# Optimization experiments

Measured on AMD Instinct MI355X. Metric: run time of the kernel, lower is better.

The kernel has to match this reference:

```python
import jax, jax.numpy as jnp
import numpy as np

N_NODES = 20000
N_EDGES = 320000
N_GRAPHS = 64


def gat_conv(x, src, dst, W, a_src, a_dst, bias, heads, ch, concat):
    # x: [N, F_in]; W: [F_in, heads*ch]; a_src/a_dst: [heads, ch]
    N = x.shape[0]
    h = (x @ W).reshape(N, heads, ch)                       # [N, H, C]
    alpha_s = jnp.sum(h * a_src, axis=-1)                   # [N, H]
    alpha_d = jnp.sum(h * a_dst, axis=-1)                   # [N, H]
    e = jax.nn.leaky_relu(alpha_s[src] + alpha_d[dst], 0.2) # [E, H]
    # segment softmax over incoming edges of each destination node
    m = jax.ops.segment_max(e, dst, num_segments=N)         # [N, H]
    ex = jnp.exp(e - m[dst])
    denom = jax.ops.segment_sum(ex, dst, num_segments=N)    # [N, H]
    alpha = ex / (denom[dst] + 1e-16)                       # [E, H]
    msg = h[src] * alpha[:, :, None]                        # [E, H, C]
    out = jax.ops.segment_sum(msg, dst, num_segments=N)     # [N, H, C]
    out = out.reshape(N, heads * ch) if concat else out.mean(axis=1)
    return out + bias, alpha


def setup_inputs() -> dict:
    key = jax.random.key(0)
    ks = jax.random.split(key, 24)
    dim_in, md, dim_out = 8, 64, 128
    hid = md * 4  # 256
    p = lambda k, shape: jax.random.normal(k, shape, dtype=jnp.float32) * 0.1
    inp = {
        "x_ppi": jax.random.normal(ks[0], (N_NODES, dim_in), dtype=jnp.float32),
        "ppi_edge_index": jax.random.randint(ks[1], (2, N_EDGES), 0, N_NODES),
        "ppi_batch": jnp.sort(jax.random.randint(ks[2], (N_NODES,), 0, N_GRAPHS)),
        # GATConv 1: dim_in -> 64, heads=4, concat
        "W1": p(ks[3], (dim_in, 4 * md)), "a_src1": p(ks[4], (4, md)), "a_dst1": p(ks[5], (4, md)), "b_gat1": jnp.zeros((hid,), jnp.float32),
        "lw1": p(ks[6], (dim_in, hid)), "lb1": jnp.zeros((hid,), jnp.float32),
        # GATConv 2: 256 -> 64, heads=4, concat
        "W2": p(ks[7], (hid, 4 * md)), "a_src2": p(ks[8], (4, md)), "a_dst2": p(ks[9], (4, md)), "b_gat2": jnp.zeros((hid,), jnp.float32),
        "lw2": p(ks[10], (hid, hid)), "lb2": jnp.zeros((hid,), jnp.float32),
        # GATConv 3: 256 -> 128, heads=6, concat=False (mean)
        "W3": p(ks[11], (hid, 6 * dim_out)), "a_src3": p(ks[12], (6, dim_out)), "a_dst3": p(ks[13], (6, dim_out)), "b_gat3": jnp.zeros((dim_out,), jnp.float32),
        "lw3": p(ks[14], (hid, dim_out)), "lb3": jnp.zeros((dim_out,), jnp.float32),
        # BatchNorm1d(dim_out), training-mode batch statistics
        "bn_gamma": jnp.ones((dim_out,), jnp.float32), "bn_beta": jnp.zeros((dim_out,), jnp.float32),
    }
    return inp


def reference(x_ppi, ppi_edge_index, ppi_batch,
              W1, a_src1, a_dst1, b_gat1, lw1, lb1,
              W2, a_src2, a_dst2, b_gat2, lw2, lb2,
              W3, a_src3, a_dst3, b_gat3, lw3, lb3,
              bn_gamma, bn_beta):
    src, dst = ppi_edge_index[0], ppi_edge_index[1]
    g1, _ = gat_conv(x_ppi, src, dst, W1, a_src1, a_dst1, b_gat1, heads=4, ch=64, concat=True)
    x = jax.nn.relu(g1 + x_ppi @ lw1 + lb1)
    g2, _ = gat_conv(x, src, dst, W2, a_src2, a_dst2, b_gat2, heads=4, ch=64, concat=True)
    x = jax.nn.relu(g2 + x @ lw2 + lb2)
    x_res = x @ lw3 + lb3
    g3, att = gat_conv(x, src, dst, W3, a_src3, a_dst3, b_gat3, heads=6, ch=128, concat=False)
    x = g3 + x_res
    x = jax.nn.relu(x)
    # BatchNorm1d, training mode (biased variance, eps=1e-5)
    mu = x.mean(axis=0)
    var = jnp.mean((x - mu) ** 2, axis=0)
    x = (x - mu) * jax.lax.rsqrt(var + 1e-5) * bn_gamma + bn_beta
    # global max pool over graphs
    pooled = jax.ops.segment_max(x, ppi_batch, num_segments=N_GRAPHS)
    return pooled, att
```

## Files before the change

### kernel.cpp

```cpp
#include <hip/hip_runtime.h>
#include <hip/hip_bf16.h>
#include <math.h>

#define N_NODES 20000
#define N_EDGES 320000
#define N_GRAPHS 64

typedef __bf16 bf16_t;
typedef bf16_t bf16x8 __attribute__((ext_vector_type(8)));
typedef bf16_t bf16x4 __attribute__((ext_vector_type(4)));
typedef bf16_t bf16x2 __attribute__((ext_vector_type(2)));
typedef float f32x4 __attribute__((ext_vector_type(4)));
typedef float f32x2 __attribute__((ext_vector_type(2)));

__global__ void hist_k(const int* __restrict__ dst, int* __restrict__ deg, int E) {
    int e = blockIdx.x * 256 + threadIdx.x;
    if (e < E) atomicAdd(&deg[dst[e]], 1);
}

__global__ __launch_bounds__(1024) void scan_k(const int* __restrict__ deg,
                                               int* __restrict__ offs,
                                               int* __restrict__ cursor, int n) {
    __shared__ int s_ws[16];
    int tid = threadIdx.x;
    int lane = tid & 63, w = tid >> 6;
    int carry = 0;
    for (int base = 0; base < n; base += 1024) {
        int i = base + tid;
        int v = (i < n) ? deg[i] : 0;
        int x = v;
        #pragma unroll
        for (int off = 1; off < 64; off <<= 1) {
            int t = __shfl_up(x, off);
            if (lane >= off) x += t;
        }
        if (lane == 63) s_ws[w] = x;
        __syncthreads();
        if (tid < 16) {
            int y = s_ws[tid];
            #pragma unroll
            for (int off = 1; off < 16; off <<= 1) {
                int t = __shfl_up(y, off);
                if (tid >= off) y += t;
            }
            s_ws[tid] = y;
        }
        __syncthreads();
        int wbase = (w > 0) ? s_ws[w - 1] : 0;
        int ex = carry + wbase + x - v;
        if (i < n) { offs[i] = ex; cursor[i] = ex; }
        carry += s_ws[15];
        __syncthreads();
    }
    if (tid == 0) offs[n] = carry;
}

__global__ void scatter_k(const int* __restrict__ src, const int* __restrict__ dst,
                          int* __restrict__ cursor, int* __restrict__ csr_src,
                          int* __restrict__ csr_eid, int E) {
    int e = blockIdx.x * 256 + threadIdx.x;
    if (e < E) {
        int d = dst[e];
        int p = atomicAdd(&cursor[d], 1);
        csr_src[p] = src[e];
        csr_eid[p] = e;
    }
}

__global__ __launch_bounds__(256) void wt_k(const float* __restrict__ W,
                                            bf16_t* __restrict__ Bt, int K, int N) {
    __shared__ float t[32][33];
    int k0 = blockIdx.y * 32, n0 = blockIdx.x * 32;
    int tx = threadIdx.x & 31, ty = threadIdx.x >> 5;
    for (int i = ty; i < 32; i += 8) t[i][tx] = W[(size_t)(k0 + i) * N + n0 + tx];
    __syncthreads();
    for (int i = ty; i < 32; i += 8)
        Bt[(size_t)(n0 + i) * K + k0 + tx] = (bf16_t)t[tx][i];
}

__global__ void w3s_k(const float* __restrict__ W3, const float* __restrict__ lw3,
                      bf16_t* __restrict__ Bt) {
    int id = blockIdx.x * 256 + threadIdx.x;
    if (id >= 128 * 1792) return;
    int n = id / 1792, k = id - n * 1792;
    float v;
    if (k < 1536) {
        int h = k >> 8, c = k & 255;
        v = W3[(size_t)c * 768 + h * 128 + n] * (1.f / 6.f);
    } else {
        int c = k - 1536;
        v = lw3[(size_t)c * 128 + n];
    }
    Bt[id] = (bf16_t)v;
}

__global__ void b40_k(const float* __restrict__ W1, const float* __restrict__ lw1,
                      float* __restrict__ B) {
    int id = blockIdx.x * 256 + threadIdx.x;
    if (id >= 40 * 256) return;
    int k = id >> 8, n = id & 255;
    float v;
    if (k < 32) {
        int h = k >> 3, c = k & 7;
        v = ((n >> 6) == h) ? W1[(size_t)c * 256 + n] : 0.f;
    } else {
        int c = k - 32;
        v = lw1[(size_t)c * 256 + n];
    }
    B[id] = v;
}

__global__ void va_k(const float* __restrict__ W, const float* __restrict__ a_s,
                     const float* __restrict__ a_d, float* __restrict__ Va,
                     float* __restrict__ Vd, int H, int C) {
    int k = blockIdx.x;
    int lane = threadIdx.x;
    const float* wr = W + (size_t)k * H * C;
    for (int h = 0; h < H; ++h) {
        float sa = 0.f, sd = 0.f;
        for (int c = lane; c < C; c += 64) {
            float wv = wr[h * C + c];
            sa += wv * a_s[h * C + c];
            sd += wv * a_d[h * C + c];
        }
        #pragma unroll
        for (int m = 32; m; m >>= 1) { sa += __shfl_xor(sa, m); sd += __shfl_xor(sd, m); }
        if (lane == 0) { Va[k * H + h] = sa; Vd[k * H + h] = sd; }
    }
}

__global__ void addb_k(const float* __restrict__ a, const float* __restrict__ b,
                       float* __restrict__ o, int n) {
    int i = blockIdx.x * 256 + threadIdx.x;
    if (i < n) o[i] = a[i] + b[i];
}

template <typename OUT>
__global__ __launch_bounds__(256) void gemm_k(const float* __restrict__ A,
                                              const float* __restrict__ B,
                                              OUT* __restrict__ C,
                                              const float* __restrict__ bias,
                                              int M, int N, int K, int relu) {
    __shared__ float As[16][65];
    __shared__ float Bs[16][64];
    int tid = threadIdx.x;
    int tx = tid & 15, ty = tid >> 4;
    int row0 = blockIdx.y * 64, col0 = blockIdx.x * 64;
    float acc[4][4] = {};
    for (int k0 = 0; k0 < K; k0 += 16) {
        #pragma unroll
        for (int i = 0; i < 4; ++i) {
            int idx = tid + i * 256;
            int m = idx >> 4, kk = idx & 15;
            int gm = row0 + m, gk = k0 + kk;
            As[kk][m] = (gm < M && gk < K) ? A[(size_t)gm * K + gk] : 0.f;
        }
        #pragma unroll
        for (int i = 0; i < 4; ++i) {
            int idx = tid + i * 256;
            int kk = idx >> 6, n = idx & 63;
            int gk = k0 + kk, gn = col0 + n;
            Bs[kk][n] = (gk < K && gn < N) ? B[(size_t)gk * N + gn] : 0.f;
        }
        __syncthreads();
        #pragma unroll
        for (int kk = 0; kk < 16; ++kk) {
            float a[4], b[4];
            #pragma unroll
            for (int i = 0; i < 4; ++i) a[i] = As[kk][ty * 4 + i];
            #pragma unroll
            for (int j = 0; j < 4; ++j) b[j] = Bs[kk][tx * 4 + j];
            #pragma unroll
            for (int i = 0; i < 4; ++i)
                #pragma unroll
                for (int j = 0; j < 4; ++j) acc[i][j] += a[i] * b[j];
        }
        __syncthreads();
    }
    #pragma unroll
    for (int i = 0; i < 4; ++i) {
        int gm = row0 + ty * 4 + i;
        if (gm >= M) continue;
        #pragma unroll
        for (int j = 0; j < 4; ++j) {
            int gn = col0 + tx * 4 + j;
            if (gn < N) {
                float r = acc[i][j] + (bias ? bias[gn] : 0.f);
                if (relu) r = fmaxf(r, 0.f);
                C[(size_t)gm * N + gn] = (OUT)r;
            }
        }
    }
}

template <typename OUT>
__global__ __launch_bounds__(256) void gemm_bf16_k(
    const bf16_t* __restrict__ A, const bf16_t* __restrict__ Bt,
    OUT* __restrict__ C, const float* __restrict__ bias, int M, int N, int K,
    const float* __restrict__ asv, const float* __restrict__ adv,
    float* __restrict__ as_o, float* __restrict__ ad_o, int H, int Ch, int relu) {
    __shared__ bf16_t As[128][40];
    __shared__ bf16_t Bs[128][40];
    int tid = threadIdx.x;
    int row0 = blockIdx.y * 128, col0 = blockIdx.x * 128;
    int wave = tid >> 6, lane = tid & 63, quad = lane >> 4, l16 = lane & 15;
    int wm = wave >> 1, wn = wave & 1;
    f32x4 acc[4][4] = {};
    int sr = tid >> 2;
    int sc = (tid & 3) * 8;
    for (int k0 = 0; k0 < K; k0 += 32) {
        #pragma unroll
        for (int half = 0; half < 2; ++half) {
            int r = sr + half * 64;
            int gm = row0 + r;
            bf16x8 v = {};
            if (gm < M) v = *(const bf16x8*)&A[(size_t)gm * K + k0 + sc];
            *(bf16x8*)&As[r][sc] = v;
            int gn = col0 + r;
            bf16x8 w = {};
            if (gn < N) w = *(const bf16x8*)&Bt[(size_t)gn * K + k0 + sc];
            *(bf16x8*)&Bs[r][sc] = w;
        }
        __syncthreads();
        bf16x8 af[4], bfr[4];
        #pragma unroll
        for (int i = 0; i < 4; ++i) {
            af[i] = *(const bf16x8*)&As[wm * 64 + i * 16 + l16][quad * 8];
            bfr[i] = *(const bf16x8*)&Bs[wn * 64 + i * 16 + l16][quad * 8];
        }
        #pragma unroll
        for (int i = 0; i < 4; ++i)
            #pragma unroll
            for (int j = 0; j < 4; ++j)
                acc[i][j] = __builtin_amdgcn_mfma_f32_16x16x32_bf16(af[i], bfr[j],
                                                                   acc[i][j], 0, 0, 0);
        __syncthreads();
    }
    #pragma unroll
    for (int i = 0; i < 4; ++i) {
        int base_m = row0 + wm * 64 + i * 16 + quad * 4;
        #pragma unroll
        for (int j = 0; j < 4; ++j) {
            int gn = col0 + wn * 64 + j * 16 + l16;
            float bv = bias ? bias[gn] : 0.f;
            #pragma unroll
            for (int r = 0; r < 4; ++r) {
                int gm = base_m + r;
                if (gm < M) {
                    float rr = acc[i][j][r] + bv;
                    if (relu) rr = fmaxf(rr, 0.f);
                    C[(size_t)gm * N + gn] = (OUT)rr;
                }
            }
        }
    }
    if (asv) {
        int hd = (col0 + wn * 64) / Ch;
        float av[4], dv[4];
        #pragma unroll
        for (int j = 0; j < 4; ++j) {
            int ca = col0 + wn * 64 + j * 16 + l16;
            av[j] = asv[ca];
            dv[j] = adv[ca];
        }
        #pragma unroll
        for (int i = 0; i < 4; ++i) {
            float sp[4] = {}, sd[4] = {};
            #pragma unroll
            for (int j = 0; j < 4; ++j)
                #pragma unroll
                for (int r = 0; r < 4; ++r) {
                    sp[r] += acc[i][j][r] * av[j];
                    sd[r] += acc[i][j][r] * dv[j];
                }
            #pragma unroll
            for (int m = 1; m < 16; m <<= 1)
                #pragma unroll
                for (int r = 0; r < 4; ++r) {
                    sp[r] += __shfl_xor(sp[r], m);
                    sd[r] += __shfl_xor(sd[r], m);
                }
            if (l16 == 0) {
                #pragma unroll
                for (int r = 0; r < 4; ++r) {
                    int gm = row0 + wm * 64 + i * 16 + quad * 4 + r;
                    if (gm < M) {
                        as_o[gm * H + hd] = sp[r];
                        ad_o[gm * H + hd] = sd[r];
                    }
                }
            }
        }
    }
}

__device__ __forceinline__ float leaky02(float v) { return v > 0.f ? v : 0.2f * v; }

__global__ void asad1_k(const float* __restrict__ x, const float* __restrict__ Va,
                        const float* __restrict__ Vd, float* __restrict__ as_,
                        float* __restrict__ ad_, int N) {
    int idx = blockIdx.x * 256 + threadIdx.x;
    if (idx >= N * 4) return;
    int j = idx >> 2, h = idx & 3;
    const float* xr = x + (size_t)j * 8;
    float sa = 0.f, sd = 0.f;
    #pragma unroll
    for (int c = 0; c < 8; ++c) {
        sa += xr[c] * Va[c * 4 + h];
        sd += xr[c] * Vd[c * 4 + h];
    }
    as_[idx] = sa;
    ad_[idx] = sd;
}

__global__ void asad3_k(const bf16_t* __restrict__ xb, const float* __restrict__ Va,
                        const float* __restrict__ Vd, float* __restrict__ as_,
                        float* __restrict__ ad_) {
    int j = blockIdx.x;
    int lane = threadIdx.x;
    bf16x4 v = *(const bf16x4*)&xb[(size_t)j * 256 + lane * 4];
    float sa[6] = {}, sd[6] = {};
    #pragma unroll
    for (int i = 0; i < 4; ++i) {
        int k = lane * 4 + i;
        float xv = (float)v[i];
        #pragma unroll
        for (int h = 0; h < 6; ++h) {
            sa[h] += xv * Va[k * 6 + h];
            sd[h] += xv * Vd[k * 6 + h];
        }
    }
    #pragma unroll
    for (int h = 0; h < 6; ++h) {
        float a = sa[h], d = sd[h];
        #pragma unroll
        for (int m = 32; m; m >>= 1) { a += __shfl_xor(a, m); d += __shfl_xor(d, m); }
        if (lane == 0) { as_[j * 6 + h] = a; ad_[j * 6 + h] = d; }
    }
}

__global__ __launch_bounds__(256) void agg_z1_k(
    const float* __restrict__ x, const float* __restrict__ as_,
    const float* __restrict__ ad_, const int* __restrict__ offs,
    const int* __restrict__ csr_src, float* __restrict__ z1) {
    int j = blockIdx.x * 4 + (threadIdx.x >> 6);
    int t = threadIdx.x & 63;
    int e_l = t >> 3, c = t & 7;
    int o0 = offs[j], deg = offs[j + 1] - o0;
    float adj0 = ad_[j * 4 + 0], adj1 = ad_[j * 4 + 1];
    float adj2 = ad_[j * 4 + 2], adj3 = ad_[j * 4 + 3];
    float acc[4] = {}, ws[4] = {};
    for (int e0 = 0; e0 < deg; e0 += 8) {
        int ne = min(8, deg - e0);
        if (e_l < ne) {
            int s = csr_src[o0 + e0 + e_l];
            float xv = x[(size_t)s * 8 + c];
            f32x4 a = *(const f32x4*)&as_[s * 4];
            float w0 = __expf(leaky02(a[0] + adj0));
            float w1 = __expf(leaky02(a[1] + adj1));
            float w2 = __expf(leaky02(a[2] + adj2));
            float w3 = __expf(leaky02(a[3] + adj3));
            acc[0] += w0 * xv; acc[1] += w1 * xv;
            acc[2] += w2 * xv; acc[3] += w3 * xv;
            ws[0] += w0; ws[1] += w1; ws[2] += w2; ws[3] += w3;
        }
    }
    #pragma unroll
    for (int m = 8; m < 64; m <<= 1)
        #pragma unroll
        for (int h = 0; h < 4; ++h) {
            acc[h] += __shfl_xor(acc[h], m);
            ws[h] += __shfl_xor(ws[h], m);
        }
    if (e_l == 0) {
        #pragma unroll
        for (int h = 0; h < 4; ++h)
            z1[(size_t)j * 40 + h * 8 + c] = acc[h] / (ws[h] + 1e-16f);
        z1[(size_t)j * 40 + 32 + c] = x[(size_t)j * 8 + c];
    }
}

__global__ __launch_bounds__(256) void agg_concat_k(
    const bf16_t* __restrict__ h, const float* __restrict__ as_,
    const float* __restrict__ ad_, const int* __restrict__ offs,
    const int* __restrict__ csr_src, const float* __restrict__ lin,
    const float* __restrict__ bgat, bf16_t* __restrict__ xb) {
    int j = blockIdx.x;
    int tid = threadIdx.x;
    int o0 = offs[j], deg = offs[j + 1] - o0;
    __shared__ int s_src[64];
    __shared__ float s_adj[4];
    __shared__ float s_ws[8][4];
    __shared__ float s_inv[4];
    __shared__ float s_red[8][256];
    if (tid < 4) s_adj[tid] = ad_[j * 4 + tid];
    int g = tid >> 5;
    int u = tid & 31;
    int myh = u >> 3;
    const char* hbase = (const char*)h + u * 16;
    f32x4 acc0 = {}, acc1 = {};
    float wsum = 0.f;
    for (int e0 = 0; e0 < deg; e0 += 64) {
        int ne = min(64, deg - e0);
        if (tid < ne) s_src[tid] = csr_src[o0 + e0 + tid];
        __syncthreads();
        float adj = s_adj[myh];
        #pragma unroll 2
        for (int e = g; e < ne; e += 8) {
            int s = s_src[e];
            float w = __expf(leaky02(as_[s * 4 + myh] + adj));
            bf16x8 v = *(const bf16x8*)(hbase + (size_t)s * 512);
            wsum += w;
            #pragma unroll
            for (int i = 0; i < 4; ++i) acc0[i] += w * (float)v[i];
            #pragma unroll
            for (int i = 0; i < 4; ++i) acc1[i] += w * (float)v[4 + i];
        }
        __syncthreads();
    }
    if ((u & 7) == 0) s_ws[g][myh] = wsum;
    *(f32x4*)&s_red[g][u * 8] = acc0;
    *(f32x4*)&s_red[g][u * 8 + 4] = acc1;
    __syncthreads();
    if (tid < 4) {
        float d = 0.f;
        #pragma unroll
        for (int g2 = 0; g2 < 8; ++g2) d += s_ws[g2][tid];
        s_inv[tid] = 1.f / (d + 1e-16f);
    }
    __syncthreads();
    {
        int c = tid;
        float s = 0.f;
        #pragma unroll
        for (int g2 = 0; g2 < 8; ++g2) s += s_red[g2][c];
        float v = fmaxf(s * s_inv[c >> 6] + bgat[c] + lin[(size_t)j * 256 + c], 0.f);
        xb[(size_t)j * 256 + c] = (bf16_t)v;
    }
}

__global__ __launch_bounds__(256) void agg_z3_k(
    const bf16_t* __restrict__ xb, const float* __restrict__ as_,
    const float* __restrict__ ad_, const int* __restrict__ offs,
    const int* __restrict__ csr_src, const int* __restrict__ csr_eid,
    bf16_t* __restrict__ z, float* __restrict__ att) {
    int j = blockIdx.x;
    int tid = threadIdx.x;
    int o0 = offs[j], deg = offs[j + 1] - o0;
    __shared__ float s_adj[6], s_denom[6], s_inv[6];
    __shared__ int s_src[64];
    __shared__ float s_w[64 * 6];
    __shared__ float s_red[8][6][256];
    if (tid < 6) { s_adj[tid] = ad_[j * 6 + tid]; s_denom[tid] = 0.f; }
    __syncthreads();
    int g = tid >> 5;
    int c = tid & 31;
    const char* xbase = (const char*)xb + c * 16;
    f32x4 a0[6] = {}, a1[6] = {};
    for (int e0 = 0; e0 < deg; e0 += 64) {
        int ne = min(64, deg - e0);
        #pragma unroll
        for (int base = 0; base < 2; ++base) {
            int idx = tid + base * 256;
            if (idx < ne * 6) {
                int e = idx / 6, h = idx - e * 6;
                int s = csr_src[o0 + e0 + e];
                if (h == 0) s_src[e] = s;
                s_w[idx] = __expf(leaky02(as_[s * 6 + h] + s_adj[h]));
            }
        }
        __syncthreads();
        if (tid < 6) {
            float d = 0.f;
            for (int e = 0; e < ne; ++e) d += s_w[e * 6 + tid];
            s_denom[tid] += d;
        }
        for (int e = g; e < ne; e += 8) {
            int s = s_src[e];
            bf16x8 v = *(const bf16x8*)(xbase + (size_t)s * 512);
            float f0[4], f1[4];
            #pragma unroll
            for (int i = 0; i < 4; ++i) { f0[i] = (float)v[i]; f1[i] = (float)v[4 + i]; }
            #pragma unroll
            for (int h = 0; h < 6; ++h) {
                float w = s_w[e * 6 + h];
                #pragma unroll
                for (int i = 0; i < 4; ++i) {
                    a0[h][i] += w * f0[i];
                    a1[h][i] += w * f1[i];
                }
            }
        }
        __syncthreads();
    }
    #pragma unroll
    for (int h = 0; h < 6; ++h) {
        *(f32x4*)&s_red[g][h][c * 8] = a0[h];
        *(f32x4*)&s_red[g][h][c * 8 + 4] = a1[h];
    }
    if (tid < 6) s_inv[tid] = 1.f / (s_denom[tid] + 1e-16f);
    __syncthreads();
    {
        int cc = tid;
        #pragma unroll
        for (int h = 0; h < 6; ++h) {
            float s = 0.f;
            #pragma unroll
            for (int g2 = 0; g2 < 8; ++g2) s += s_red[g2][h][cc];
            z[(size_t)j * 1792 + h * 256 + cc] = (bf16_t)(s * s_inv[h]);
        }
    }
    if (tid < 32)
        *(bf16x8*)&z[(size_t)j * 1792 + 1536 + tid * 8] =
            *(const bf16x8*)&xb[(size_t)j * 256 + tid * 8];
    for (int idx = tid; idx < deg * 6; idx += 256) {
        int e = idx / 6, h = idx - e * 6;
        int p = o0 + e;
        int s = csr_src[p];
        att[(size_t)csr_eid[p] * 6 + h] =
            __expf(leaky02(as_[s * 6 + h] + s_adj[h])) * s_inv[h];
    }
}

__global__ void bn_stats_k(const float* __restrict__ y, float* __restrict__ sums, int N) {
    int c = threadIdx.x;
    float s = 0.f, q = 0.f;
    for (int r = blockIdx.x; r < N; r += gridDim.x) {
        float v = y[(size_t)r * 128 + c];
        s += v;
        q += v * v;
    }
    atomicAdd(&sums[c], s);
    atomicAdd(&sums[128 + c], q);
}
__global__ void bn_scale_k(const float* __restrict__ sums, const float* __restrict__ gamma,
                           const float* __restrict__ beta, float* __restrict__ scale,
                           float* __restrict__ shift, int N) {
    int c = threadIdx.x;
    float mu = sums[c] / (float)N;
    float var = fmaxf(sums[128 + c] / (float)N - mu * mu, 0.f);
    float inv = rsqrtf(var + 1e-5f) * gamma[c];
    scale[c] = inv;
    shift[c] = beta[c] - mu * inv;
}

__device__ __forceinline__ unsigned f2key(float f) {
    unsigned b = __float_as_uint(f);
    return (b & 0x80000000u) ? ~b : (b | 0x80000000u);
}
__global__ void pool_init_k(unsigned* __restrict__ pool_u) {
    int i = blockIdx.x * 256 + threadIdx.x;
    if (i < N_GRAPHS * 128) pool_u[i] = f2key(-3.402823466e38f * 2.0f);
}
__global__ void norm_pool_k(const float* __restrict__ y, const float* __restrict__ scale,
                            const float* __restrict__ shift, const int* __restrict__ batch,
                            unsigned* __restrict__ pool_u, int N) {
    int idx = blockIdx.x * 256 + threadIdx.x;
    if (idx >= N * 128) return;
    int n = idx >> 7, c = idx & 127;
    float v = y[idx] * scale[c] + shift[c];
    atomicMax(&pool_u[batch[n] * 128 + c], f2key(v));
}
__global__ void pool_write_k(const unsigned* __restrict__ pool_u, float* __restrict__ out) {
    int i = blockIdx.x * 256 + threadIdx.x;
    if (i < N_GRAPHS * 128) {
        unsigned u = pool_u[i];
        unsigned b = (u & 0x80000000u) ? (u & 0x7FFFFFFFu) : ~u;
        out[i] = __uint_as_float(b);
    }
}

extern "C" void kernel_launch(void* const* d_in, const int* in_sizes, int n_in,
                              void* d_out, int out_size, void* d_ws, size_t ws_size,
                              hipStream_t stream) {
    const int N = N_NODES, E = N_EDGES;
    const float* x_ppi = (const float*)d_in[0];
    const int* edge = (const int*)d_in[1];
    const int* batch = (const int*)d_in[2];
    const float* W1 = (const float*)d_in[3];
    const float* a_src1 = (const float*)d_in[4];
    const float* a_dst1 = (const float*)d_in[5];
    const float* b_gat1 = (const float*)d_in[6];
    const float* lw1 = (const float*)d_in[7];
    const float* lb1 = (const float*)d_in[8];
    const float* W2 = (const float*)d_in[9];
    const float* a_src2 = (const float*)d_in[10];
    const float* a_dst2 = (const float*)d_in[11];
    const float* b_gat2 = (const float*)d_in[12];
    const float* lw2 = (const float*)d_in[13];
    const float* lb2 = (const float*)d_in[14];
    const float* W3 = (const float*)d_in[15];
    const float* a_src3 = (const float*)d_in[16];
    const float* a_dst3 = (const float*)d_in[17];
    const float* b_gat3 = (const float*)d_in[18];
    const float* lw3 = (const float*)d_in[19];
    const float* lb3 = (const float*)d_in[20];
    const float* bn_gamma = (const float*)d_in[21];
    const float* bn_beta = (const float*)d_in[22];

    const int* src = edge;
    const int* dst = edge + E;

    size_t off = 0;
    auto alloc = [&](size_t bytes) {
        size_t o = off;
        off = (off + bytes + 255) & ~(size_t)255;
        return o;
    };
    char* ws = (char*)d_ws;
    bf16_t* xb = (bf16_t*)(ws + alloc((size_t)N * 256 * 2));
    bf16_t* zbig = (bf16_t*)(ws + alloc((size_t)N * 1792 * 2));
    bf16_t* hb = zbig;
    bf16_t* z3 = zbig;
    float* lin = (float*)(ws + alloc((size_t)N * 256 * 4));
    float* z1 = (float*)(ws + alloc((size_t)N * 40 * 4));
    float* as_ = (float*)(ws + alloc((size_t)N * 6 * 4));
    float* ad_ = (float*)(ws + alloc((size_t)N * 6 * 4));
    int* deg = (int*)(ws + alloc((size_t)(N + 1) * 4));
    int* offs = (int*)(ws + alloc((size_t)(N + 1) * 4));
    int* cursor = (int*)(ws + alloc((size_t)(N + 1) * 4));
    int* csr_src = (int*)(ws + alloc((size_t)E * 4));
    int* csr_eid = (int*)(ws + alloc((size_t)E * 4));
    bf16_t* Wt2 = (bf16_t*)(ws + alloc((size_t)256 * 256 * 2));
    bf16_t* lwt2 = (bf16_t*)(ws + alloc((size_t)256 * 256 * 2));
    bf16_t* Bt3s = (bf16_t*)(ws + alloc((size_t)128 * 1792 * 2));
    float* B40 = (float*)(ws + alloc((size_t)40 * 256 * 4));
    float* Va1 = (float*)(ws + alloc(8 * 4 * 4));
    float* Vd1 = (float*)(ws + alloc(8 * 4 * 4));
    float* Va3 = (float*)(ws + alloc(256 * 6 * 4));
    float* Vd3 = (float*)(ws + alloc(256 * 6 * 4));
    float* bias1s = (float*)(ws + alloc(256 * 4));
    float* bias3s = (float*)(ws + alloc(128 * 4));
    float* bn_sums = (float*)(ws + alloc(256 * 4));
    float* bn_scale = (float*)(ws + alloc(128 * 4));
    float* bn_shift = (float*)(ws + alloc(128 * 4));
    unsigned* pool_u = (unsigned*)(ws + alloc((size_t)N_GRAPHS * 128 * 4));

    float* out_pool = (float*)d_out;
    float* out_att = (float*)d_out + N_GRAPHS * 128;

    hipMemsetAsync(deg, 0, (size_t)N * 4, stream);
    hist_k<<<(E + 255) / 256, 256, 0, stream>>>(dst, deg, E);
    scan_k<<<1, 1024, 0, stream>>>(deg, offs, cursor, N);
    scatter_k<<<(E + 255) / 256, 256, 0, stream>>>(src, dst, cursor, csr_src, csr_eid, E);
    wt_k<<<dim3(8, 8), 256, 0, stream>>>(W2, Wt2, 256, 256);
    wt_k<<<dim3(8, 8), 256, 0, stream>>>(lw2, lwt2, 256, 256);
    w3s_k<<<896, 256, 0, stream>>>(W3, lw3, Bt3s);
    b40_k<<<40, 256, 0, stream>>>(W1, lw1, B40);
    va_k<<<8, 64, 0, stream>>>(W1, a_src1, a_dst1, Va1, Vd1, 4, 64);
    va_k<<<256, 64, 0, stream>>>(W3, a_src3, a_dst3, Va3, Vd3, 6, 128);
    addb_k<<<1, 256, 0, stream>>>(lb1, b_gat1, bias1s, 256);
    addb_k<<<1, 128, 0, stream>>>(lb3, b_gat3, bias3s, 128);

    asad1_k<<<(N * 4 + 255) / 256, 256, 0, stream>>>(x_ppi, Va1, Vd1, as_, ad_, N);
    agg_z1_k<<<N / 4, 256, 0, stream>>>(x_ppi, as_, ad_, offs, csr_src, z1);
    gemm_k<bf16_t><<<dim3(4, 313), 256, 0, stream>>>(z1, B40, xb, bias1s, N, 256, 40, 1);

    gemm_bf16_k<bf16_t><<<dim3(2, 157), 256, 0, stream>>>(xb, Wt2, hb, nullptr, N, 256, 256,
                                                          a_src2, a_dst2, as_, ad_, 4, 64, 0);
    gemm_bf16_k<float><<<dim3(2, 157), 256, 0, stream>>>(xb, lwt2, lin, lb2, N, 256, 256,
                                                         nullptr, nullptr, nullptr, nullptr,
                                                         0, 1, 0);
    agg_concat_k<<<N, 256, 0, stream>>>(hb, as_, ad_, offs, csr_src, lin, b_gat2, xb);

    asad3_k<<<N, 64, 0, stream>>>(xb, Va3, Vd3, as_, ad_);
    agg_z3_k<<<N, 256, 0, stream>>>(xb, as_, ad_, offs, csr_src, csr_eid, z3, out_att);
    float* y = lin;
    gemm_bf16_k<float><<<dim3(1, 157), 256, 0, stream>>>(z3, Bt3s, y, bias3s, N, 128, 1792,
                                                         nullptr, nullptr, nullptr, nullptr,
                                                         0, 1, 1);

    hipMemsetAsync(bn_sums, 0, 256 * 4, stream);
    bn_stats_k<<<160, 128, 0, stream>>>(y, bn_sums, N);
    bn_scale_k<<<1, 128, 0, stream>>>(bn_sums, bn_gamma, bn_beta, bn_scale, bn_shift, N);

    pool_init_k<<<(N_GRAPHS * 128 + 255) / 256, 256, 0, stream>>>(pool_u);
    norm_pool_k<<<((size_t)N * 128 + 255) / 256, 256, 0, stream>>>(y, bn_scale, bn_shift, batch,
                                                                   pool_u, N);
    pool_write_k<<<(N_GRAPHS * 128 + 255) / 256, 256, 0, stream>>>(pool_u, out_pool);
}
```

Measured before the change: 567.0 us.

## Assign one warp per head in layer-3 aggregation, removing shared-memory reduction

Restructures agg_z3_k so each of 6 wavefront-sized groups handles one attention head across all incoming edges, instead of 8 edge groups each accumulating all 6 heads. This drops the 48KB shared reduction buffer and its extra pass and sync, cuts per-thread registers, and lets the softmax denominator be summed per thread. In exchange, each source feature row is loaded by six groups rather than one, relying on cache reuse, and each edge loop runs serially over all edges per group, lengthening the per-block critical path.

```diff
diff --git a/kernel.cpp b/kernel.cpp
--- a/kernel.cpp
+++ b/kernel.cpp
@@ -439,7 +439,7 @@
     }
 }
 
-__global__ __launch_bounds__(256) void agg_z3_k(
+__global__ __launch_bounds__(192) void agg_z3_k(
     const bf16_t* __restrict__ xb, const float* __restrict__ as_,
     const float* __restrict__ ad_, const int* __restrict__ offs,
     const int* __restrict__ csr_src, const int* __restrict__ csr_eid,
@@ -447,78 +447,63 @@
     int j = blockIdx.x;
     int tid = threadIdx.x;
     int o0 = offs[j], deg = offs[j + 1] - o0;
-    __shared__ float s_adj[6], s_denom[6], s_inv[6];
+    __shared__ float s_adj[6];
     __shared__ int s_src[64];
     __shared__ float s_w[64 * 6];
-    __shared__ float s_red[8][6][256];
-    if (tid < 6) { s_adj[tid] = ad_[j * 6 + tid]; s_denom[tid] = 0.f; }
+    __shared__ float s_inv[6];
+    if (tid < 6) s_adj[tid] = ad_[j * 6 + tid];
     __syncthreads();
-    int g = tid >> 5;
+    int h = tid >> 5;
     int c = tid & 31;
     const char* xbase = (const char*)xb + c * 16;
-    f32x4 a0[6] = {}, a1[6] = {};
+    f32x4 a0 = {}, a1 = {};
+    float wsum = 0.f;
     for (int e0 = 0; e0 < deg; e0 += 64) {
         int ne = min(64, deg - e0);
         #pragma unroll
         for (int base = 0; base < 2; ++base) {
-            int idx = tid + base * 256;
+            int idx = tid + base * 192;
             if (idx < ne * 6) {
-                int e = idx / 6, h = idx - e * 6;
+                int e = idx / 6, hh = idx - e * 6;
                 int s = csr_src[o0 + e0 + e];
-                if (h == 0) s_src[e] = s;
-                s_w[idx] = __expf(leaky02(as_[s * 6 + h] + s_adj[h]));
+                if (hh == 0) s_src[e] = s;
+                s_w[idx] = __expf(leaky02(as_[s * 6 + hh] + s_adj[hh]));
             }
         }
         __syncthreads();
-        if (tid < 6) {
-            float d = 0.f;
-            for (int e = 0; e < ne; ++e) d += s_w[e * 6 + tid];
-            s_denom[tid] += d;
-        }
-        for (int e = g; e < ne; e += 8) {
+        #pragma unroll 4
+        for (int e = 0; e < ne; ++e) {
             int s = s_src[e];
+            float w = s_w[e * 6 + h];
             bf16x8 v = *(const bf16x8*)(xbase + (size_t)s * 512);
-            float f0[4], f1[4];
-            #pragma unroll
-            for (int i = 0; i < 4; ++i) { f0[i] = (float)v[i]; f1[i] = (float)v[4 + i]; }
-            #pragma unroll
-            for (int h = 0; h < 6; ++h) {
-                float w = s_w[e * 6 + h];
-                #pragma unroll
-                for (int i = 0; i < 4; ++i) {
-                    a0[h][i] += w * f0[i];
-                    a1[h][i] += w * f1[i];
-                }
-            }
-        }
-        __syncthreads();
-    }
-    #pragma unroll
-    for (int h = 0; h < 6; ++h) {
-        *(f32x4*)&s_red[g][h][c * 8] = a0[h];
-        *(f32x4*)&s_red[g][h][c * 8 + 4] = a1[h];
-    }
-    if (tid < 6) s_inv[tid] = 1.f / (s_denom[tid] + 1e-16f);
-    __syncthreads();
+            wsum += w;
+            #pragma unroll
+            for (int i = 0; i < 4; ++i) a0[i] += w * (float)v[i];
+            #pragma unroll
+            for (int i = 0; i < 4; ++i) a1[i] += w * (float)v[4 + i];
+        }
+        __syncthreads();
+    }
+    float inv = 1.f / (wsum + 1e-16f);
     {
-        int cc = tid;
-        #pragma unroll
-        for (int h = 0; h < 6; ++h) {
-            float s = 0.f;
-            #pragma unroll
-            for (int g2 = 0; g2 < 8; ++g2) s += s_red[g2][h][cc];
-            z[(size_t)j * 1792 + h * 256 + cc] = (bf16_t)(s * s_inv[h]);
-        }
+        bf16x8 o;
+        #pragma unroll
+        for (int i = 0; i < 4; ++i) o[i] = (bf16_t)(a0[i] * inv);
+        #pragma unroll
+        for (int i = 0; i < 4; ++i) o[4 + i] = (bf16_t)(a1[i] * inv);
+        *(bf16x8*)&z[(size_t)j * 1792 + h * 256 + c * 8] = o;
     }
     if (tid < 32)
         *(bf16x8*)&z[(size_t)j * 1792 + 1536 + tid * 8] =
             *(const bf16x8*)&xb[(size_t)j * 256 + tid * 8];
-    for (int idx = tid; idx < deg * 6; idx += 256) {
-        int e = idx / 6, h = idx - e * 6;
+    if (c == 0) s_inv[h] = inv;
+    __syncthreads();
+    for (int idx = tid; idx < deg * 6; idx += 192) {
+        int e = idx / 6, hh = idx - e * 6;
         int p = o0 + e;
         int s = csr_src[p];
-        att[(size_t)csr_eid[p] * 6 + h] =
-            __expf(leaky02(as_[s * 6 + h] + s_adj[h])) * s_inv[h];
+        att[(size_t)csr_eid[p] * 6 + hh] =
+            __expf(leaky02(as_[s * 6 + hh] + s_adj[hh])) * s_inv[hh];
     }
 }
 
@@ -664,7 +649,7 @@
     agg_concat_k<<<N, 256, 0, stream>>>(hb, as_, ad_, offs, csr_src, lin, b_gat2, xb);
 
     asad3_k<<<N, 64, 0, stream>>>(xb, Va3, Vd3, as_, ad_);
-    agg_z3_k<<<N, 256, 0, stream>>>(xb, as_, ad_, offs, csr_src, csr_eid, z3, out_att);
+    agg_z3_k<<<N, 192, 0, stream>>>(xb, as_, ad_, offs, csr_src, csr_eid, z3, out_att);
     float* y = lin;
     gemm_bf16_k<float><<<dim3(1, 157), 256, 0, stream>>>(z3, Bt3s, y, bias3s, N, 128, 1792,
                                                          nullptr, nullptr, nullptr, nullptr,
```

Result: faster. 494.7 us (-12.8%).
